# Kernel optimization log

Hardware: AMD Instinct MI355X
Metric: run time of the kernel (lower is better)

The kernel has to match this reference:

```python
import jax, jax.numpy as jnp
import numpy as np

N, E = 100000, 1600000          # nodes, edges
IN_N, IN_E = 128, 32            # input node / edge feature dims
OUT_N, OUT_E, H = 32, 16, 4     # per-head output dims, num heads


def setup_inputs() -> dict:
    key = jax.random.key(0)
    ks = jax.random.split(key, 10)
    s = 0.05
    return {
        "n_feats": jax.random.normal(ks[0], (N, IN_N), jnp.float32),
        "e_feats": jax.random.normal(ks[1], (E, IN_E), jnp.float32),
        "src": jax.random.randint(ks[2], (E,), 0, N),
        "dst": jax.random.randint(ks[3], (E,), 0, N),
        "W_ni": jax.random.normal(ks[4], (IN_N, H * OUT_E), jnp.float32) * s,
        "W_nj": jax.random.normal(ks[5], (IN_N, H * OUT_E), jnp.float32) * s,
        "W_fij": jax.random.normal(ks[6], (IN_E, H * OUT_E), jnp.float32) * s,
        "bias_e": jnp.zeros((H * OUT_E,), jnp.float32),
        "attn": jax.random.normal(ks[7], (H, OUT_E), jnp.float32) * s,
        "W_node": jax.random.normal(ks[8], (IN_N, H * OUT_N), jnp.float32) * s,
    }


def reference(n_feats, e_feats, src, dst, W_ni, W_nj, W_fij, bias_e, attn, W_node):
    num_nodes = n_feats.shape[0]
    # Dense projections (small GEMMs)
    f_ni = n_feats @ W_ni          # [N, H*OUT_E]
    f_nj = n_feats @ W_nj          # [N, H*OUT_E]
    f_fij = e_feats @ W_fij        # [E, H*OUT_E]
    # Edge features: gather src/dst node projections onto edges
    f_out = f_ni[src] + f_nj[dst] + f_fij + bias_e
    f_out = jax.nn.leaky_relu(f_out, 0.01).reshape(-1, H, OUT_E)  # [E,H,OUT_E]
    # Attention logits per edge per head
    e = jnp.einsum('ehf,hf->eh', f_out, attn)  # [E, H]
    # Edge softmax: normalize over incoming edges of each dst node
    m = jax.ops.segment_max(e, dst, num_segments=num_nodes)   # [N, H]
    ex = jnp.exp(e - m[dst])
    s = jax.ops.segment_sum(ex, dst, num_segments=num_nodes)  # [N, H]
    a = ex / s[dst]                                           # [E, H]
    # Node output: weighted sum of src node projections over incoming edges
    h = (n_feats @ W_node).reshape(-1, H, OUT_N)              # [N, H, OUT_N]
    msg = h[src] * a[:, :, None]                              # [E, H, OUT_N]
    h_out = jax.ops.segment_sum(msg, dst, num_segments=num_nodes)  # [N,H,OUT_N]
    return h_out, f_out
```

## Files before the change

### kernel.cpp

```cpp
#include <hip/hip_runtime.h>
#include <hip/hip_bf16.h>
#include <math.h>

#define NH 4
#define OE 16
#define ON 32
#define INN 128
#define INE 32
#define HOE 64
#define HON 128

typedef __attribute__((ext_vector_type(8))) short bf16x8;
typedef __attribute__((ext_vector_type(4))) float f32x4;

__device__ __forceinline__ unsigned cvt_pk_bf16(float lo, float hi) {
    unsigned r;
    asm volatile("v_cvt_pk_bf16_f32 %0, %1, %2" : "=v"(r) : "v"(lo), "v"(hi));
    return r;
}

__global__ void k_zero_i32(int* __restrict__ p, int n) {
    int i = blockIdx.x * blockDim.x + threadIdx.x;
    int stride = gridDim.x * blockDim.x;
    for (; i < n; i += stride) p[i] = 0;
}

__global__ void k_count(const int* __restrict__ dst, int* __restrict__ count, int Ee) {
    int i = blockIdx.x * blockDim.x + threadIdx.x;
    int stride = gridDim.x * blockDim.x;
    for (; i < Ee; i += stride) atomicAdd(&count[dst[i]], 1);
}

__launch_bounds__(256)
__global__ void k_node_gemm(const float* __restrict__ nf,
                            const float* __restrict__ Wni,
                            const float* __restrict__ Wnj,
                            const float* __restrict__ Wnode,
                            float* __restrict__ fni,
                            float* __restrict__ fnj,
                            float* __restrict__ hproj,
                            int Nn) {
    int tid = threadIdx.x;
    int lane = tid & 63;
    int w = tid >> 6;
    int m = lane & 15;
    int kq = lane >> 4;
    const float* W; float* out; int wstride, wcoff, ostride, ocoff;
    if (w == 0)      { W = Wni;   wstride = 64;  wcoff = 0;  out = fni;   ostride = 64;  ocoff = 0; }
    else if (w == 1) { W = Wnj;   wstride = 64;  wcoff = 0;  out = fnj;   ostride = 64;  ocoff = 0; }
    else if (w == 2) { W = Wnode; wstride = 128; wcoff = 0;  out = hproj; ostride = 128; ocoff = 0; }
    else             { W = Wnode; wstride = 128; wcoff = 64; out = hproj; ostride = 128; ocoff = 64; }
    bf16x8 bv[4][4];
    #pragma unroll
    for (int k32 = 0; k32 < 4; k32++) {
        #pragma unroll
        for (int t = 0; t < 4; t++) {
            unsigned* bw = (unsigned*)&bv[k32][t];
            #pragma unroll
            for (int i = 0; i < 4; i++) {
                int k0 = k32 * 32 + kq * 8 + 2 * i;
                float lo = W[(size_t)k0 * wstride + wcoff + t * 16 + m];
                float hi = W[(size_t)(k0 + 1) * wstride + wcoff + t * 16 + m];
                bw[i] = cvt_pk_bf16(lo, hi);
            }
        }
    }
    int ngroups = (Nn + 15) >> 4;
    for (int g = blockIdx.x; g < ngroups; g += gridDim.x) {
        int r0 = g << 4;
        int ra = r0 + m; if (ra >= Nn) ra = Nn - 1;
        const float* ap = &nf[(size_t)ra * INN + kq * 8];
        bf16x8 av[4];
        #pragma unroll
        for (int k32 = 0; k32 < 4; k32++) {
            float4 a0 = *(const float4*)(ap + k32 * 32);
            float4 a1 = *(const float4*)(ap + k32 * 32 + 4);
            unsigned* aw = (unsigned*)&av[k32];
            aw[0] = cvt_pk_bf16(a0.x, a0.y);
            aw[1] = cvt_pk_bf16(a0.z, a0.w);
            aw[2] = cvt_pk_bf16(a1.x, a1.y);
            aw[3] = cvt_pk_bf16(a1.z, a1.w);
        }
        f32x4 c[4];
        #pragma unroll
        for (int t = 0; t < 4; t++) {
            c[t] = (f32x4){0.f, 0.f, 0.f, 0.f};
            #pragma unroll
            for (int k32 = 0; k32 < 4; k32++)
                c[t] = __builtin_amdgcn_mfma_f32_16x16x32_bf16(av[k32], bv[k32][t], c[t], 0, 0, 0);
        }
        #pragma unroll
        for (int t = 0; t < 4; t++) {
            #pragma unroll
            for (int j = 0; j < 4; j++) {
                int gr = r0 + kq * 4 + j;
                if (gr < Nn) out[(size_t)gr * ostride + ocoff + t * 16 + m] = c[t][j];
            }
        }
    }
}

__launch_bounds__(256)
__global__ void k_edge(const float* __restrict__ efeats,
                       const int* __restrict__ src,
                       const int* __restrict__ dst,
                       const float* __restrict__ Wfij,
                       const float* __restrict__ bias,
                       const float* __restrict__ attn,
                       const float* __restrict__ fni,
                       const float* __restrict__ fnj,
                       const int* __restrict__ offsets,
                       int* __restrict__ cursor,
                       int* __restrict__ eids,
                       float* __restrict__ fout,
                       float* __restrict__ exws,
                       int Ee) {
    int tid = threadIdx.x;
    int lane = tid & 63;
    int m = lane & 15;
    int kq = lane >> 4;
    bf16x8 bv[4];
    #pragma unroll
    for (int t = 0; t < 4; t++) {
        unsigned* bw = (unsigned*)&bv[t];
        #pragma unroll
        for (int i = 0; i < 4; i++) {
            float lo = Wfij[(kq * 8 + 2 * i) * HOE + t * 16 + m];
            float hi = Wfij[(kq * 8 + 2 * i + 1) * HOE + t * 16 + m];
            bw[i] = cvt_pk_bf16(lo, hi);
        }
    }
    float bb[4], aa[4];
    #pragma unroll
    for (int t = 0; t < 4; t++) { bb[t] = bias[t * 16 + m]; aa[t] = attn[t * 16 + m]; }

    int wid = (blockIdx.x * 256 + tid) >> 6;
    int nw = (gridDim.x * 256) >> 6;
    for (int e0 = wid * 16; e0 < Ee; e0 += nw * 16) {
        int ea = e0 + m; if (ea >= Ee) ea = Ee - 1;
        const float* ap = &efeats[(size_t)ea * INE + kq * 8];
        float4 a0 = *(const float4*)ap;
        float4 a1 = *(const float4*)(ap + 4);
        int eq[4], sj[4], dj[4]; bool ok[4];
        #pragma unroll
        for (int j = 0; j < 4; j++) {
            int q = e0 + kq * 4 + j;
            ok[j] = q < Ee;
            int ec = ok[j] ? q : (Ee - 1);
            eq[j] = q; sj[j] = src[ec]; dj[j] = dst[ec];
        }
        float gni[4][4], gnj[4][4];
        #pragma unroll
        for (int j = 0; j < 4; j++) {
            const float* pi = &fni[(size_t)sj[j] * HOE + m];
            const float* pj = &fnj[(size_t)dj[j] * HOE + m];
            #pragma unroll
            for (int t = 0; t < 4; t++) {
                gni[j][t] = pi[t * 16];
                gnj[j][t] = pj[t * 16];
            }
        }
        bf16x8 av;
        {
            unsigned* aw = (unsigned*)&av;
            aw[0] = cvt_pk_bf16(a0.x, a0.y);
            aw[1] = cvt_pk_bf16(a0.z, a0.w);
            aw[2] = cvt_pk_bf16(a1.x, a1.y);
            aw[3] = cvt_pk_bf16(a1.z, a1.w);
        }
        f32x4 c[4];
        #pragma unroll
        for (int t = 0; t < 4; t++) {
            c[t] = __builtin_amdgcn_mfma_f32_16x16x32_bf16(av, bv[t], (f32x4){0.f,0.f,0.f,0.f}, 0, 0, 0);
        }
        #pragma unroll
        for (int j = 0; j < 4; j++) {
            #pragma unroll
            for (int t = 0; t < 4; t++) {
                int col = t * 16 + m;
                float fv = c[t][j] + gni[j][t] + gnj[j][t] + bb[t];
                fv = fv > 0.f ? fv : 0.01f * fv;
                if (ok[j]) fout[(size_t)eq[j] * HOE + col] = fv;
                float pl = fv * aa[t];
                #pragma unroll
                for (int o = 8; o >= 1; o >>= 1) pl += __shfl_xor(pl, o, 16);
                if (ok[j] && m == 0) exws[(size_t)eq[j] * NH + t] = __expf(pl);
            }
            if (ok[j] && m == 0) {
                int p = atomicAdd(&cursor[dj[j]], 1);
                eids[offsets[dj[j]] + p] = eq[j];
            }
        }
    }
}

__global__ void k_scan_chunks(const int* __restrict__ count,
                              int* __restrict__ chunkscan,
                              int* __restrict__ chunktot, int n) {
    __shared__ int tmp[256];
    int t = threadIdx.x;
    int i = blockIdx.x * 256 + t;
    int v = (i < n) ? count[i] : 0;
    tmp[t] = v;
    __syncthreads();
    for (int o = 1; o < 256; o <<= 1) {
        int x = (t >= o) ? tmp[t - o] : 0;
        __syncthreads();
        tmp[t] += x;
        __syncthreads();
    }
    if (i < n) chunkscan[i] = tmp[t] - v;
    if (t == 255) chunktot[blockIdx.x] = tmp[t];
}

__global__ void k_scan_tot(const int* __restrict__ tot, int* __restrict__ base, int nc) {
    __shared__ int tmp[1024];
    int t = threadIdx.x;
    int v = (t < nc) ? tot[t] : 0;
    tmp[t] = v;
    __syncthreads();
    for (int o = 1; o < 1024; o <<= 1) {
        int x = (t >= o) ? tmp[t - o] : 0;
        __syncthreads();
        tmp[t] += x;
        __syncthreads();
    }
    if (t < nc) base[t] = tmp[t] - v;
}

__global__ void k_offsets(const int* __restrict__ chunkscan,
                          const int* __restrict__ chunkbase,
                          int* __restrict__ offsets, int Nn, int Ee) {
    int i = blockIdx.x * blockDim.x + threadIdx.x;
    if (i < Nn) offsets[i] = chunkscan[i] + chunkbase[i >> 8];
    if (i == 0) offsets[Nn] = Ee;
}

__launch_bounds__(256)
__global__ void k_node_out(const int* __restrict__ offsets,
                           const int* __restrict__ eids,
                           const int* __restrict__ srcv,
                           const float* __restrict__ exws,
                           const float* __restrict__ hproj,
                           float* __restrict__ hout,
                           int Nn) {
    int lane = threadIdx.x & 63;
    int n = (blockIdx.x * 256 + threadIdx.x) >> 6;
    if (n >= Nn) return;
    int o0 = offsets[n], o1 = offsets[n + 1];
    int hi = lane >> 5;
    float s0 = 0.f, s1 = 0.f, s2 = 0.f, s3 = 0.f;
    float a0 = 0.f, a1 = 0.f;
    for (int i0 = o0; i0 < o1; i0 += 64) {
        int nb = min(64, o1 - i0);
        int ve = 0, vs = 0;
        if (lane < nb) {
            ve = eids[i0 + lane];
            vs = srcv[ve];
        }
        for (int j = 0; j < nb; j++) {
            int e = __builtin_amdgcn_readlane(ve, j);
            int s = __builtin_amdgcn_readlane(vs, j);
            float4 x = *(const float4*)&exws[(size_t)e * NH];
            s0 += x.x; s1 += x.y; s2 += x.z; s3 += x.w;
            float exl = (hi == 0) ? x.x : x.y;
            float exh = (hi == 0) ? x.z : x.w;
            a0 += hproj[(size_t)s * HON + lane] * exl;
            a1 += hproj[(size_t)s * HON + 64 + lane] * exh;
        }
    }
    float r0 = s0 > 0.f ? 1.f / s0 : 0.f;
    float r1 = s1 > 0.f ? 1.f / s1 : 0.f;
    float r2 = s2 > 0.f ? 1.f / s2 : 0.f;
    float r3 = s3 > 0.f ? 1.f / s3 : 0.f;
    float rlo = (hi == 0) ? r0 : r1;
    float rhi = (hi == 0) ? r2 : r3;
    hout[(size_t)n * HON + lane] = a0 * rlo;
    hout[(size_t)n * HON + 64 + lane] = a1 * rhi;
}

extern "C" void kernel_launch(void* const* d_in, const int* in_sizes, int n_in,
                              void* d_out, int out_size, void* d_ws, size_t ws_size,
                              hipStream_t stream) {
    const float* n_feats = (const float*)d_in[0];
    const float* e_feats = (const float*)d_in[1];
    const int*   src     = (const int*)d_in[2];
    const int*   dst     = (const int*)d_in[3];
    const float* W_ni    = (const float*)d_in[4];
    const float* W_nj    = (const float*)d_in[5];
    const float* W_fij   = (const float*)d_in[6];
    const float* bias_e  = (const float*)d_in[7];
    const float* attn    = (const float*)d_in[8];
    const float* W_node  = (const float*)d_in[9];

    const int Nn = in_sizes[0] / INN;
    const int Ee = in_sizes[2];

    float* hout = (float*)d_out;
    float* fout = (float*)d_out + (size_t)Nn * HON;

    char* ws = (char*)d_ws;
    size_t off = 0;
    auto alloc = [&](size_t bytes) {
        size_t o = off;
        off = (off + bytes + 255) & ~(size_t)255;
        return o;
    };
    size_t o_fni   = alloc((size_t)Nn * HOE * 4);
    size_t o_fnj   = alloc((size_t)Nn * HOE * 4);
    size_t o_hproj = alloc((size_t)Nn * HON * 4);
    size_t o_exws  = alloc((size_t)Ee * NH * 4);
    size_t o_eids  = alloc((size_t)Ee * 4);
    size_t o_cnt2  = alloc((size_t)2 * Nn * 4);
    size_t o_offs  = alloc((size_t)(Nn + 1) * 4);
    size_t o_cscan = alloc((size_t)Nn * 4);
    size_t o_cbase = alloc((size_t)1024 * 4);
    (void)ws_size;

    float* fni   = (float*)(ws + o_fni);
    float* fnj   = (float*)(ws + o_fnj);
    float* hproj = (float*)(ws + o_hproj);
    float* exws  = (float*)(ws + o_exws);
    int* eids    = (int*)(ws + o_eids);
    int* cnt2    = (int*)(ws + o_cnt2);
    int* count   = cnt2;
    int* cursor  = cnt2 + Nn;
    int* offsets = (int*)(ws + o_offs);
    int* cscan   = (int*)(ws + o_cscan);
    int* cbase   = (int*)(ws + o_cbase);

    int nchunks = (Nn + 255) / 256;

    k_zero_i32<<<(2 * Nn + 255) / 256, 256, 0, stream>>>(cnt2, 2 * Nn);

    k_count<<<2048, 256, 0, stream>>>(dst, count, Ee);

    k_node_gemm<<<1024, 256, 0, stream>>>(
        n_feats, W_ni, W_nj, W_node, fni, fnj, hproj, Nn);

    k_scan_chunks<<<nchunks, 256, 0, stream>>>(count, cscan, cbase, Nn);
    k_scan_tot<<<1, 1024, 0, stream>>>(cbase, cbase, nchunks);
    k_offsets<<<(Nn + 255) / 256, 256, 0, stream>>>(cscan, cbase, offsets, Nn, Ee);

    k_edge<<<8192, 256, 0, stream>>>(
        e_feats, src, dst, W_fij, bias_e, attn, fni, fnj,
        offsets, cursor, eids, fout, exws, Ee);

    k_node_out<<<(Nn + 3) / 4, 256, 0, stream>>>(
        offsets, eids, src, exws, hproj, hout, Nn);
}
```

Baseline: 642.4 us.

## Software-pipeline edge kernel, interleave hproj layout, batch node-out gathers

The edge kernel now gives each wave a fixed set of four tiles. It preloads src/dst indices for all of them and double-buffers the edge-feature and fni/fnj gathers for the next tile while computing the current one. It also swaps the shuffle reduction for DPP row sums, uses nontemporal loads and stores, and sizes the grid to match. The node GEMM writes hproj interleaved so node_out can fetch both heads' values with one float2 load, and node_out unrolls four edges at a time to expose more memory-level parallelism. The extra buffers raise register pressure, and the edge grid becomes much smaller, which can lower occupancy.

```diff
diff --git a/kernel.cpp b/kernel.cpp
--- a/kernel.cpp
+++ b/kernel.cpp
@@ -17,6 +17,19 @@
     unsigned r;
     asm volatile("v_cvt_pk_bf16_f32 %0, %1, %2" : "=v"(r) : "v"(lo), "v"(hi));
     return r;
+}
+
+__device__ __forceinline__ float rowsum16(float v) {
+    int x;
+    x = __builtin_amdgcn_update_dpp(0, __float_as_int(v), 0x128, 0xf, 0xf, true);
+    v += __int_as_float(x);
+    x = __builtin_amdgcn_update_dpp(0, __float_as_int(v), 0x124, 0xf, 0xf, true);
+    v += __int_as_float(x);
+    x = __builtin_amdgcn_update_dpp(0, __float_as_int(v), 0x122, 0xf, 0xf, true);
+    v += __int_as_float(x);
+    x = __builtin_amdgcn_update_dpp(0, __float_as_int(v), 0x121, 0xf, 0xf, true);
+    v += __int_as_float(x);
+    return v;
 }
 
 __global__ void k_zero_i32(int* __restrict__ p, int n) {
@@ -45,11 +58,12 @@
     int w = tid >> 6;
     int m = lane & 15;
     int kq = lane >> 4;
-    const float* W; float* out; int wstride, wcoff, ostride, ocoff;
-    if (w == 0)      { W = Wni;   wstride = 64;  wcoff = 0;  out = fni;   ostride = 64;  ocoff = 0; }
-    else if (w == 1) { W = Wnj;   wstride = 64;  wcoff = 0;  out = fnj;   ostride = 64;  ocoff = 0; }
-    else if (w == 2) { W = Wnode; wstride = 128; wcoff = 0;  out = hproj; ostride = 128; ocoff = 0; }
-    else             { W = Wnode; wstride = 128; wcoff = 64; out = hproj; ostride = 128; ocoff = 64; }
+    const float* W; float* out; int wstride, wcoff, ostride;
+    int omul, oadd;
+    if (w == 0)      { W = Wni;   wstride = 64;  wcoff = 0;  out = fni;   ostride = 64;  omul = 1; oadd = 0; }
+    else if (w == 1) { W = Wnj;   wstride = 64;  wcoff = 0;  out = fnj;   ostride = 64;  omul = 1; oadd = 0; }
+    else if (w == 2) { W = Wnode; wstride = 128; wcoff = 0;  out = hproj; ostride = 128; omul = 2; oadd = 0; }
+    else             { W = Wnode; wstride = 128; wcoff = 64; out = hproj; ostride = 128; omul = 2; oadd = 1; }
     bf16x8 bv[4][4];
     #pragma unroll
     for (int k32 = 0; k32 < 4; k32++) {
@@ -73,13 +87,13 @@
         bf16x8 av[4];
         #pragma unroll
         for (int k32 = 0; k32 < 4; k32++) {
-            float4 a0 = *(const float4*)(ap + k32 * 32);
-            float4 a1 = *(const float4*)(ap + k32 * 32 + 4);
+            f32x4 a0 = *(const f32x4*)(ap + k32 * 32);
+            f32x4 a1 = *(const f32x4*)(ap + k32 * 32 + 4);
             unsigned* aw = (unsigned*)&av[k32];
-            aw[0] = cvt_pk_bf16(a0.x, a0.y);
-            aw[1] = cvt_pk_bf16(a0.z, a0.w);
-            aw[2] = cvt_pk_bf16(a1.x, a1.y);
-            aw[3] = cvt_pk_bf16(a1.z, a1.w);
+            aw[0] = cvt_pk_bf16(a0[0], a0[1]);
+            aw[1] = cvt_pk_bf16(a0[2], a0[3]);
+            aw[2] = cvt_pk_bf16(a1[0], a1[1]);
+            aw[3] = cvt_pk_bf16(a1[2], a1[3]);
         }
         f32x4 c[4];
         #pragma unroll
@@ -94,12 +108,14 @@
             #pragma unroll
             for (int j = 0; j < 4; j++) {
                 int gr = r0 + kq * 4 + j;
-                if (gr < Nn) out[(size_t)gr * ostride + ocoff + t * 16 + m] = c[t][j];
-            }
-        }
-    }
-}
-
+                int col = t * 16 + m;
+                if (gr < Nn) out[(size_t)gr * ostride + col * omul + oadd] = c[t][j];
+            }
+        }
+    }
+}
+
+#define MAXT 4
 __launch_bounds__(256)
 __global__ void k_edge(const float* __restrict__ efeats,
                        const int* __restrict__ src,
@@ -135,60 +151,99 @@
     for (int t = 0; t < 4; t++) { bb[t] = bias[t * 16 + m]; aa[t] = attn[t * 16 + m]; }
 
     int wid = (blockIdx.x * 256 + tid) >> 6;
-    int nw = (gridDim.x * 256) >> 6;
-    for (int e0 = wid * 16; e0 < Ee; e0 += nw * 16) {
-        int ea = e0 + m; if (ea >= Ee) ea = Ee - 1;
+    int nw = gridDim.x * 4;
+    int ntiles = (Ee + 15) >> 4;
+
+    int sj[MAXT][4], dj[MAXT][4];
+    #pragma unroll
+    for (int it = 0; it < MAXT; it++) {
+        int T = wid + it * nw;
+        #pragma unroll
+        for (int j = 0; j < 4; j++) {
+            int e = T * 16 + kq * 4 + j;
+            int ec = (T < ntiles && e < Ee) ? e : 0;
+            sj[it][j] = src[ec];
+            dj[it][j] = dst[ec];
+        }
+    }
+
+    f32x4 araw[2][2];
+    float gni[2][4][4], gnj[2][4][4];
+
+    if (wid < ntiles) {
+        int ea = wid * 16 + m; if (ea >= Ee) ea = Ee - 1;
         const float* ap = &efeats[(size_t)ea * INE + kq * 8];
-        float4 a0 = *(const float4*)ap;
-        float4 a1 = *(const float4*)(ap + 4);
-        int eq[4], sj[4], dj[4]; bool ok[4];
+        araw[0][0] = __builtin_nontemporal_load((const f32x4*)ap);
+        araw[0][1] = __builtin_nontemporal_load((const f32x4*)(ap + 4));
         #pragma unroll
         for (int j = 0; j < 4; j++) {
-            int q = e0 + kq * 4 + j;
-            ok[j] = q < Ee;
-            int ec = ok[j] ? q : (Ee - 1);
-            eq[j] = q; sj[j] = src[ec]; dj[j] = dst[ec];
-        }
-        float gni[4][4], gnj[4][4];
-        #pragma unroll
-        for (int j = 0; j < 4; j++) {
-            const float* pi = &fni[(size_t)sj[j] * HOE + m];
-            const float* pj = &fnj[(size_t)dj[j] * HOE + m];
+            const float* pi = &fni[(size_t)sj[0][j] * HOE + m];
+            const float* pj = &fnj[(size_t)dj[0][j] * HOE + m];
             #pragma unroll
             for (int t = 0; t < 4; t++) {
-                gni[j][t] = pi[t * 16];
-                gnj[j][t] = pj[t * 16];
-            }
-        }
-        bf16x8 av;
-        {
-            unsigned* aw = (unsigned*)&av;
-            aw[0] = cvt_pk_bf16(a0.x, a0.y);
-            aw[1] = cvt_pk_bf16(a0.z, a0.w);
-            aw[2] = cvt_pk_bf16(a1.x, a1.y);
-            aw[3] = cvt_pk_bf16(a1.z, a1.w);
-        }
-        f32x4 c[4];
-        #pragma unroll
-        for (int t = 0; t < 4; t++) {
-            c[t] = __builtin_amdgcn_mfma_f32_16x16x32_bf16(av, bv[t], (f32x4){0.f,0.f,0.f,0.f}, 0, 0, 0);
-        }
-        #pragma unroll
-        for (int j = 0; j < 4; j++) {
+                gni[0][j][t] = pi[t * 16];
+                gnj[0][j][t] = pj[t * 16];
+            }
+        }
+    }
+
+    #pragma unroll
+    for (int it = 0; it < MAXT; it++) {
+        int T = wid + it * nw;
+        if (T < ntiles) {
+            const int cur = it & 1, nxt = cur ^ 1;
+            if (it + 1 < MAXT) {
+                int Tn = T + nw;
+                if (Tn < ntiles) {
+                    int ea = Tn * 16 + m; if (ea >= Ee) ea = Ee - 1;
+                    const float* ap = &efeats[(size_t)ea * INE + kq * 8];
+                    araw[nxt][0] = __builtin_nontemporal_load((const f32x4*)ap);
+                    araw[nxt][1] = __builtin_nontemporal_load((const f32x4*)(ap + 4));
+                    const int itn = (it + 1 < MAXT) ? it + 1 : 0;
+                    #pragma unroll
+                    for (int j = 0; j < 4; j++) {
+                        const float* pi = &fni[(size_t)sj[itn][j] * HOE + m];
+                        const float* pj = &fnj[(size_t)dj[itn][j] * HOE + m];
+                        #pragma unroll
+                        for (int t = 0; t < 4; t++) {
+                            gni[nxt][j][t] = pi[t * 16];
+                            gnj[nxt][j][t] = pj[t * 16];
+                        }
+                    }
+                }
+            }
+            bf16x8 av;
+            {
+                unsigned* aw = (unsigned*)&av;
+                aw[0] = cvt_pk_bf16(araw[cur][0][0], araw[cur][0][1]);
+                aw[1] = cvt_pk_bf16(araw[cur][0][2], araw[cur][0][3]);
+                aw[2] = cvt_pk_bf16(araw[cur][1][0], araw[cur][1][1]);
+                aw[3] = cvt_pk_bf16(araw[cur][1][2], araw[cur][1][3]);
+            }
+            f32x4 c[4];
             #pragma unroll
             for (int t = 0; t < 4; t++) {
-                int col = t * 16 + m;
-                float fv = c[t][j] + gni[j][t] + gnj[j][t] + bb[t];
-                fv = fv > 0.f ? fv : 0.01f * fv;
-                if (ok[j]) fout[(size_t)eq[j] * HOE + col] = fv;
-                float pl = fv * aa[t];
+                c[t] = __builtin_amdgcn_mfma_f32_16x16x32_bf16(av, bv[t], (f32x4){0.f,0.f,0.f,0.f}, 0, 0, 0);
+            }
+            int e0 = T * 16;
+            #pragma unroll
+            for (int j = 0; j < 4; j++) {
+                int eq = e0 + kq * 4 + j;
+                bool ok = eq < Ee;
                 #pragma unroll
-                for (int o = 8; o >= 1; o >>= 1) pl += __shfl_xor(pl, o, 16);
-                if (ok[j] && m == 0) exws[(size_t)eq[j] * NH + t] = __expf(pl);
-            }
-            if (ok[j] && m == 0) {
-                int p = atomicAdd(&cursor[dj[j]], 1);
-                eids[offsets[dj[j]] + p] = eq[j];
+                for (int t = 0; t < 4; t++) {
+                    int col = t * 16 + m;
+                    float fv = c[t][j] + gni[cur][j][t] + gnj[cur][j][t] + bb[t];
+                    fv = fv > 0.f ? fv : 0.01f * fv;
+                    if (ok) __builtin_nontemporal_store(fv, &fout[(size_t)eq * HOE + col]);
+                    float pl = rowsum16(fv * aa[t]);
+                    if (ok && m == 0) exws[(size_t)eq * NH + t] = __expf(pl);
+                }
+                if (ok && m == 0) {
+                    int dd = dj[it][j];
+                    int p = atomicAdd(&cursor[dd], 1);
+                    eids[offsets[dd] + p] = eq;
+                }
             }
         }
     }
@@ -241,7 +296,7 @@
                            const int* __restrict__ eids,
                            const int* __restrict__ srcv,
                            const float* __restrict__ exws,
-                           const float* __restrict__ hproj,
+                           const float* __restrict__ hproj2,
                            float* __restrict__ hout,
                            int Nn) {
     int lane = threadIdx.x & 63;
@@ -258,15 +313,27 @@
             ve = eids[i0 + lane];
             vs = srcv[ve];
         }
-        for (int j = 0; j < nb; j++) {
-            int e = __builtin_amdgcn_readlane(ve, j);
-            int s = __builtin_amdgcn_readlane(vs, j);
-            float4 x = *(const float4*)&exws[(size_t)e * NH];
-            s0 += x.x; s1 += x.y; s2 += x.z; s3 += x.w;
-            float exl = (hi == 0) ? x.x : x.y;
-            float exh = (hi == 0) ? x.z : x.w;
-            a0 += hproj[(size_t)s * HON + lane] * exl;
-            a1 += hproj[(size_t)s * HON + 64 + lane] * exh;
+        for (int j0 = 0; j0 < nb; j0 += 4) {
+            int cnt = nb - j0;
+            float4 xx[4]; float2 hp[4];
+            #pragma unroll
+            for (int u = 0; u < 4; u++) {
+                int jj = j0 + ((u < cnt) ? u : cnt - 1);
+                int e = __builtin_amdgcn_readlane(ve, jj);
+                int s = __builtin_amdgcn_readlane(vs, jj);
+                xx[u] = *(const float4*)&exws[(size_t)e * NH];
+                hp[u] = *(const float2*)&hproj2[(size_t)s * HON + lane * 2];
+            }
+            #pragma unroll
+            for (int u = 0; u < 4; u++) {
+                float4 x = xx[u];
+                if (u >= cnt) x = make_float4(0.f, 0.f, 0.f, 0.f);
+                s0 += x.x; s1 += x.y; s2 += x.z; s3 += x.w;
+                float exl = (hi == 0) ? x.x : x.y;
+                float exh = (hi == 0) ? x.z : x.w;
+                a0 += hp[u].x * exl;
+                a1 += hp[u].y * exh;
+            }
         }
     }
     float r0 = s0 > 0.f ? 1.f / s0 : 0.f;
@@ -275,8 +342,8 @@
     float r3 = s3 > 0.f ? 1.f / s3 : 0.f;
     float rlo = (hi == 0) ? r0 : r1;
     float rhi = (hi == 0) ? r2 : r3;
-    hout[(size_t)n * HON + lane] = a0 * rlo;
-    hout[(size_t)n * HON + 64 + lane] = a1 * rhi;
+    __builtin_nontemporal_store(a0 * rlo, &hout[(size_t)n * HON + lane]);
+    __builtin_nontemporal_store(a1 * rhi, &hout[(size_t)n * HON + 64 + lane]);
 }
 
 extern "C" void kernel_launch(void* const* d_in, const int* in_sizes, int n_in,
@@ -330,6 +397,8 @@
     int* cbase   = (int*)(ws + o_cbase);
 
     int nchunks = (Nn + 255) / 256;
+    int ntiles = (Ee + 15) >> 4;
+    int nblk_edge = (ntiles + 15) / 16;
 
     k_zero_i32<<<(2 * Nn + 255) / 256, 256, 0, stream>>>(cnt2, 2 * Nn);
 
@@ -342,7 +411,7 @@
     k_scan_tot<<<1, 1024, 0, stream>>>(cbase, cbase, nchunks);
     k_offsets<<<(Nn + 255) / 256, 256, 0, stream>>>(cscan, cbase, offsets, Nn, Ee);
 
-    k_edge<<<8192, 256, 0, stream>>>(
+    k_edge<<<nblk_edge, 256, 0, stream>>>(
         e_feats, src, dst, W_fij, bias_e, attn, fni, fnj,
         offsets, cursor, eids, fout, exws, Ee);
 
```

New measurement: 680.8 us. +6.0%, slower.

## Build CSR before edge pass and write edge outputs in dst-sorted order

Applied to the files above, without the earlier changes.

A separate fill kernel builds the dst-sorted edge id list before the edge kernel runs. The edge kernel then walks edges in CSR order and writes exp-logits and src ids contiguously per position, so the node aggregation reads them sequentially instead of through eids indirection. The edge kernel also uses DPP row reductions instead of shuffles and float4 exp stores, and hproj is interleaved so each lane reads one float2. In exchange, the edge kernel now gathers e_feats and writes f_out in scattered order, adds an extra srcp buffer, and adds one launch.

```diff
diff --git a/kernel.cpp b/kernel.cpp
--- a/kernel.cpp
+++ b/kernel.cpp
@@ -17,6 +17,19 @@
     unsigned r;
     asm volatile("v_cvt_pk_bf16_f32 %0, %1, %2" : "=v"(r) : "v"(lo), "v"(hi));
     return r;
+}
+
+__device__ __forceinline__ float rowsum16(float v) {
+    int x;
+    x = __builtin_amdgcn_update_dpp(0, __float_as_int(v), 0x128, 0xf, 0xf, true);
+    v += __int_as_float(x);
+    x = __builtin_amdgcn_update_dpp(0, __float_as_int(v), 0x124, 0xf, 0xf, true);
+    v += __int_as_float(x);
+    x = __builtin_amdgcn_update_dpp(0, __float_as_int(v), 0x122, 0xf, 0xf, true);
+    v += __int_as_float(x);
+    x = __builtin_amdgcn_update_dpp(0, __float_as_int(v), 0x121, 0xf, 0xf, true);
+    v += __int_as_float(x);
+    return v;
 }
 
 __global__ void k_zero_i32(int* __restrict__ p, int n) {
@@ -45,11 +58,12 @@
     int w = tid >> 6;
     int m = lane & 15;
     int kq = lane >> 4;
-    const float* W; float* out; int wstride, wcoff, ostride, ocoff;
-    if (w == 0)      { W = Wni;   wstride = 64;  wcoff = 0;  out = fni;   ostride = 64;  ocoff = 0; }
-    else if (w == 1) { W = Wnj;   wstride = 64;  wcoff = 0;  out = fnj;   ostride = 64;  ocoff = 0; }
-    else if (w == 2) { W = Wnode; wstride = 128; wcoff = 0;  out = hproj; ostride = 128; ocoff = 0; }
-    else             { W = Wnode; wstride = 128; wcoff = 64; out = hproj; ostride = 128; ocoff = 64; }
+    const float* W; float* out; int wstride, wcoff, ostride;
+    int omul, oadd;
+    if (w == 0)      { W = Wni;   wstride = 64;  wcoff = 0;  out = fni;   ostride = 64;  omul = 1; oadd = 0; }
+    else if (w == 1) { W = Wnj;   wstride = 64;  wcoff = 0;  out = fnj;   ostride = 64;  omul = 1; oadd = 0; }
+    else if (w == 2) { W = Wnode; wstride = 128; wcoff = 0;  out = hproj; ostride = 128; omul = 2; oadd = 0; }
+    else             { W = Wnode; wstride = 128; wcoff = 64; out = hproj; ostride = 128; omul = 2; oadd = 1; }
     bf16x8 bv[4][4];
     #pragma unroll
     for (int k32 = 0; k32 < 4; k32++) {
@@ -73,13 +87,13 @@
         bf16x8 av[4];
         #pragma unroll
         for (int k32 = 0; k32 < 4; k32++) {
-            float4 a0 = *(const float4*)(ap + k32 * 32);
-            float4 a1 = *(const float4*)(ap + k32 * 32 + 4);
+            f32x4 a0 = *(const f32x4*)(ap + k32 * 32);
+            f32x4 a1 = *(const f32x4*)(ap + k32 * 32 + 4);
             unsigned* aw = (unsigned*)&av[k32];
-            aw[0] = cvt_pk_bf16(a0.x, a0.y);
-            aw[1] = cvt_pk_bf16(a0.z, a0.w);
-            aw[2] = cvt_pk_bf16(a1.x, a1.y);
-            aw[3] = cvt_pk_bf16(a1.z, a1.w);
+            aw[0] = cvt_pk_bf16(a0[0], a0[1]);
+            aw[1] = cvt_pk_bf16(a0[2], a0[3]);
+            aw[2] = cvt_pk_bf16(a1[0], a1[1]);
+            aw[3] = cvt_pk_bf16(a1[2], a1[3]);
         }
         f32x4 c[4];
         #pragma unroll
@@ -94,101 +108,8 @@
             #pragma unroll
             for (int j = 0; j < 4; j++) {
                 int gr = r0 + kq * 4 + j;
-                if (gr < Nn) out[(size_t)gr * ostride + ocoff + t * 16 + m] = c[t][j];
-            }
-        }
-    }
-}
-
-__launch_bounds__(256)
-__global__ void k_edge(const float* __restrict__ efeats,
-                       const int* __restrict__ src,
-                       const int* __restrict__ dst,
-                       const float* __restrict__ Wfij,
-                       const float* __restrict__ bias,
-                       const float* __restrict__ attn,
-                       const float* __restrict__ fni,
-                       const float* __restrict__ fnj,
-                       const int* __restrict__ offsets,
-                       int* __restrict__ cursor,
-                       int* __restrict__ eids,
-                       float* __restrict__ fout,
-                       float* __restrict__ exws,
-                       int Ee) {
-    int tid = threadIdx.x;
-    int lane = tid & 63;
-    int m = lane & 15;
-    int kq = lane >> 4;
-    bf16x8 bv[4];
-    #pragma unroll
-    for (int t = 0; t < 4; t++) {
-        unsigned* bw = (unsigned*)&bv[t];
-        #pragma unroll
-        for (int i = 0; i < 4; i++) {
-            float lo = Wfij[(kq * 8 + 2 * i) * HOE + t * 16 + m];
-            float hi = Wfij[(kq * 8 + 2 * i + 1) * HOE + t * 16 + m];
-            bw[i] = cvt_pk_bf16(lo, hi);
-        }
-    }
-    float bb[4], aa[4];
-    #pragma unroll
-    for (int t = 0; t < 4; t++) { bb[t] = bias[t * 16 + m]; aa[t] = attn[t * 16 + m]; }
-
-    int wid = (blockIdx.x * 256 + tid) >> 6;
-    int nw = (gridDim.x * 256) >> 6;
-    for (int e0 = wid * 16; e0 < Ee; e0 += nw * 16) {
-        int ea = e0 + m; if (ea >= Ee) ea = Ee - 1;
-        const float* ap = &efeats[(size_t)ea * INE + kq * 8];
-        float4 a0 = *(const float4*)ap;
-        float4 a1 = *(const float4*)(ap + 4);
-        int eq[4], sj[4], dj[4]; bool ok[4];
-        #pragma unroll
-        for (int j = 0; j < 4; j++) {
-            int q = e0 + kq * 4 + j;
-            ok[j] = q < Ee;
-            int ec = ok[j] ? q : (Ee - 1);
-            eq[j] = q; sj[j] = src[ec]; dj[j] = dst[ec];
-        }
-        float gni[4][4], gnj[4][4];
-        #pragma unroll
-        for (int j = 0; j < 4; j++) {
-            const float* pi = &fni[(size_t)sj[j] * HOE + m];
-            const float* pj = &fnj[(size_t)dj[j] * HOE + m];
-            #pragma unroll
-            for (int t = 0; t < 4; t++) {
-                gni[j][t] = pi[t * 16];
-                gnj[j][t] = pj[t * 16];
-            }
-        }
-        bf16x8 av;
-        {
-            unsigned* aw = (unsigned*)&av;
-            aw[0] = cvt_pk_bf16(a0.x, a0.y);
-            aw[1] = cvt_pk_bf16(a0.z, a0.w);
-            aw[2] = cvt_pk_bf16(a1.x, a1.y);
-            aw[3] = cvt_pk_bf16(a1.z, a1.w);
-        }
-        f32x4 c[4];
-        #pragma unroll
-        for (int t = 0; t < 4; t++) {
-            c[t] = __builtin_amdgcn_mfma_f32_16x16x32_bf16(av, bv[t], (f32x4){0.f,0.f,0.f,0.f}, 0, 0, 0);
-        }
-        #pragma unroll
-        for (int j = 0; j < 4; j++) {
-            #pragma unroll
-            for (int t = 0; t < 4; t++) {
                 int col = t * 16 + m;
-                float fv = c[t][j] + gni[j][t] + gnj[j][t] + bb[t];
-                fv = fv > 0.f ? fv : 0.01f * fv;
-                if (ok[j]) fout[(size_t)eq[j] * HOE + col] = fv;
-                float pl = fv * aa[t];
-                #pragma unroll
-                for (int o = 8; o >= 1; o >>= 1) pl += __shfl_xor(pl, o, 16);
-                if (ok[j] && m == 0) exws[(size_t)eq[j] * NH + t] = __expf(pl);
-            }
-            if (ok[j] && m == 0) {
-                int p = atomicAdd(&cursor[dj[j]], 1);
-                eids[offsets[dj[j]] + p] = eq[j];
+                if (gr < Nn) out[(size_t)gr * ostride + col * omul + oadd] = c[t][j];
             }
         }
     }
@@ -236,12 +157,123 @@
     if (i == 0) offsets[Nn] = Ee;
 }
 
+__global__ void k_fill(const int* __restrict__ dst,
+                       const int* __restrict__ offsets,
+                       int* __restrict__ cursor,
+                       int* __restrict__ eids, int Ee) {
+    int i = blockIdx.x * blockDim.x + threadIdx.x;
+    int stride = gridDim.x * blockDim.x;
+    for (; i < Ee; i += stride) {
+        int d = dst[i];
+        int p = atomicAdd(&cursor[d], 1);
+        eids[offsets[d] + p] = i;
+    }
+}
+
+__launch_bounds__(256)
+__global__ void k_edge(const float* __restrict__ efeats,
+                       const int* __restrict__ src,
+                       const int* __restrict__ dst,
+                       const float* __restrict__ Wfij,
+                       const float* __restrict__ bias,
+                       const float* __restrict__ attn,
+                       const float* __restrict__ fni,
+                       const float* __restrict__ fnj,
+                       const int* __restrict__ eids,
+                       float* __restrict__ fout,
+                       float* __restrict__ exwsp,
+                       int* __restrict__ srcp,
+                       int Ee) {
+    int tid = threadIdx.x;
+    int lane = tid & 63;
+    int m = lane & 15;
+    int kq = lane >> 4;
+    bf16x8 bv[4];
+    #pragma unroll
+    for (int t = 0; t < 4; t++) {
+        unsigned* bw = (unsigned*)&bv[t];
+        #pragma unroll
+        for (int i = 0; i < 4; i++) {
+            float lo = Wfij[(kq * 8 + 2 * i) * HOE + t * 16 + m];
+            float hi = Wfij[(kq * 8 + 2 * i + 1) * HOE + t * 16 + m];
+            bw[i] = cvt_pk_bf16(lo, hi);
+        }
+    }
+    float bb[4], aa[4];
+    #pragma unroll
+    for (int t = 0; t < 4; t++) { bb[t] = bias[t * 16 + m]; aa[t] = attn[t * 16 + m]; }
+
+    int wid = (blockIdx.x * 256 + tid) >> 6;
+    int nw = (gridDim.x * 256) >> 6;
+    int ntiles = (Ee + 15) >> 4;
+    for (int T = wid; T < ntiles; T += nw) {
+        int i0 = T << 4;
+        int ia = i0 + m;
+        int ra = eids[(ia < Ee) ? ia : (Ee - 1)];
+        const float* ap = &efeats[(size_t)ra * INE + kq * 8];
+        f32x4 a0 = *(const f32x4*)ap;
+        f32x4 a1 = *(const f32x4*)(ap + 4);
+        int eq[4], sj[4], dj[4]; bool ok[4];
+        #pragma unroll
+        for (int j = 0; j < 4; j++) {
+            int pos = i0 + kq * 4 + j;
+            ok[j] = pos < Ee;
+            int pc = ok[j] ? pos : (Ee - 1);
+            eq[j] = eids[pc];
+            sj[j] = src[eq[j]];
+            dj[j] = dst[eq[j]];
+        }
+        float gni[4][4], gnj[4][4];
+        #pragma unroll
+        for (int j = 0; j < 4; j++) {
+            const float* pi = &fni[(size_t)sj[j] * HOE + m];
+            const float* pj = &fnj[(size_t)dj[j] * HOE + m];
+            #pragma unroll
+            for (int t = 0; t < 4; t++) {
+                gni[j][t] = pi[t * 16];
+                gnj[j][t] = pj[t * 16];
+            }
+        }
+        bf16x8 av;
+        {
+            unsigned* aw = (unsigned*)&av;
+            aw[0] = cvt_pk_bf16(a0[0], a0[1]);
+            aw[1] = cvt_pk_bf16(a0[2], a0[3]);
+            aw[2] = cvt_pk_bf16(a1[0], a1[1]);
+            aw[3] = cvt_pk_bf16(a1[2], a1[3]);
+        }
+        f32x4 c[4];
+        #pragma unroll
+        for (int t = 0; t < 4; t++) {
+            c[t] = __builtin_amdgcn_mfma_f32_16x16x32_bf16(av, bv[t], (f32x4){0.f,0.f,0.f,0.f}, 0, 0, 0);
+        }
+        #pragma unroll
+        for (int j = 0; j < 4; j++) {
+            int pos = i0 + kq * 4 + j;
+            float pl[4];
+            #pragma unroll
+            for (int t = 0; t < 4; t++) {
+                int col = t * 16 + m;
+                float fv = c[t][j] + gni[j][t] + gnj[j][t] + bb[t];
+                fv = fv > 0.f ? fv : 0.01f * fv;
+                if (ok[j]) fout[(size_t)eq[j] * HOE + col] = fv;
+                pl[t] = rowsum16(fv * aa[t]);
+            }
+            if (ok[j] && m == 0) {
+                float4 ex = make_float4(__expf(pl[0]), __expf(pl[1]),
+                                        __expf(pl[2]), __expf(pl[3]));
+                *(float4*)&exwsp[(size_t)pos * NH] = ex;
+                srcp[pos] = sj[j];
+            }
+        }
+    }
+}
+
 __launch_bounds__(256)
 __global__ void k_node_out(const int* __restrict__ offsets,
-                           const int* __restrict__ eids,
-                           const int* __restrict__ srcv,
-                           const float* __restrict__ exws,
-                           const float* __restrict__ hproj,
+                           const int* __restrict__ srcp,
+                           const float* __restrict__ exwsp,
+                           const float* __restrict__ hproj2,
                            float* __restrict__ hout,
                            int Nn) {
     int lane = threadIdx.x & 63;
@@ -253,20 +285,28 @@
     float a0 = 0.f, a1 = 0.f;
     for (int i0 = o0; i0 < o1; i0 += 64) {
         int nb = min(64, o1 - i0);
-        int ve = 0, vs = 0;
-        if (lane < nb) {
-            ve = eids[i0 + lane];
-            vs = srcv[ve];
-        }
-        for (int j = 0; j < nb; j++) {
-            int e = __builtin_amdgcn_readlane(ve, j);
-            int s = __builtin_amdgcn_readlane(vs, j);
-            float4 x = *(const float4*)&exws[(size_t)e * NH];
-            s0 += x.x; s1 += x.y; s2 += x.z; s3 += x.w;
-            float exl = (hi == 0) ? x.x : x.y;
-            float exh = (hi == 0) ? x.z : x.w;
-            a0 += hproj[(size_t)s * HON + lane] * exl;
-            a1 += hproj[(size_t)s * HON + 64 + lane] * exh;
+        int vs = 0;
+        if (lane < nb) vs = srcp[i0 + lane];
+        for (int j0 = 0; j0 < nb; j0 += 4) {
+            int cnt = nb - j0;
+            float4 xx[4]; float2 hp[4];
+            #pragma unroll
+            for (int u = 0; u < 4; u++) {
+                int jj = j0 + ((u < cnt) ? u : cnt - 1);
+                int s = __builtin_amdgcn_readlane(vs, jj);
+                xx[u] = *(const float4*)&exwsp[(size_t)(i0 + jj) * NH];
+                hp[u] = *(const float2*)&hproj2[(size_t)s * HON + lane * 2];
+            }
+            #pragma unroll
+            for (int u = 0; u < 4; u++) {
+                float4 x = xx[u];
+                if (u >= cnt) x = make_float4(0.f, 0.f, 0.f, 0.f);
+                s0 += x.x; s1 += x.y; s2 += x.z; s3 += x.w;
+                float exl = (hi == 0) ? x.x : x.y;
+                float exh = (hi == 0) ? x.z : x.w;
+                a0 += hp[u].x * exl;
+                a1 += hp[u].y * exh;
+            }
         }
     }
     float r0 = s0 > 0.f ? 1.f / s0 : 0.f;
@@ -311,6 +351,7 @@
     size_t o_hproj = alloc((size_t)Nn * HON * 4);
     size_t o_exws  = alloc((size_t)Ee * NH * 4);
     size_t o_eids  = alloc((size_t)Ee * 4);
+    size_t o_srcp  = alloc((size_t)Ee * 4);
     size_t o_cnt2  = alloc((size_t)2 * Nn * 4);
     size_t o_offs  = alloc((size_t)(Nn + 1) * 4);
     size_t o_cscan = alloc((size_t)Nn * 4);
@@ -320,8 +361,9 @@
     float* fni   = (float*)(ws + o_fni);
     float* fnj   = (float*)(ws + o_fnj);
     float* hproj = (float*)(ws + o_hproj);
-    float* exws  = (float*)(ws + o_exws);
+    float* exwsp = (float*)(ws + o_exws);
     int* eids    = (int*)(ws + o_eids);
+    int* srcp    = (int*)(ws + o_srcp);
     int* cnt2    = (int*)(ws + o_cnt2);
     int* count   = cnt2;
     int* cursor  = cnt2 + Nn;
@@ -342,10 +384,12 @@
     k_scan_tot<<<1, 1024, 0, stream>>>(cbase, cbase, nchunks);
     k_offsets<<<(Nn + 255) / 256, 256, 0, stream>>>(cscan, cbase, offsets, Nn, Ee);
 
+    k_fill<<<4096, 256, 0, stream>>>(dst, offsets, cursor, eids, Ee);
+
     k_edge<<<8192, 256, 0, stream>>>(
         e_feats, src, dst, W_fij, bias_e, attn, fni, fnj,
-        offsets, cursor, eids, fout, exws, Ee);
+        eids, fout, exwsp, srcp, Ee);
 
     k_node_out<<<(Nn + 3) / 4, 256, 0, stream>>>(
-        offsets, eids, src, exws, hproj, hout, Nn);
-}
+        offsets, srcp, exwsp, hproj, hout, Nn);
+}
```

New measurement: 654.1 us. About the same (+1.8%).
